# Kernel optimization log

Measured on AMD Instinct MI355X. Metric: run time of the kernel, lower is better.

## Reference

```python
import jax, jax.numpy as jnp
import numpy as np

NUM_HEADS = 8


def _proj(W, b, x):
    # x: [B, C, N] channel-wise 1x1 conv == matmul over channels
    return jnp.einsum('oc,bcn->bon', W, x) + b[None, :, None]


def setup_inputs() -> dict:
    key = jax.random.key(0)
    ks = jax.random.split(key, 8)
    B, C, H, W = 4, 512, 24, 24
    inp = {
        'feat0': jax.random.normal(ks[0], (B, C, H, W), jnp.float32),
        'feat1': jax.random.normal(ks[1], (B, C, H, W), jnp.float32),
        'feat2': jax.random.normal(ks[2], (B, C, H, W), jnp.float32),
        'Wq': jax.random.normal(ks[3], (C, C), jnp.float32) * 0.02,
        'bq': jnp.zeros((C,), jnp.float32),
        'Wk': jax.random.normal(ks[4], (C, C), jnp.float32) * 0.02,
        'bk': jnp.zeros((C,), jnp.float32),
        'Wv': jax.random.normal(ks[5], (C, C), jnp.float32) * 0.02,
        'bv': jnp.zeros((C,), jnp.float32),
        'Wo': jax.random.normal(ks[6], (C, C), jnp.float32) * 0.02,
        'bo': jnp.zeros((C,), jnp.float32),
    }
    return inp


def reference(feat0, feat1, feat2, Wq, bq, Wk, bk, Wv, bv, Wo, bo):
    feats = [feat0, feat1, feat2]
    B, C, H, W = feat0.shape
    h = NUM_HEADS
    d = C // h
    scale = d ** -0.5

    # Precompute K/V once per feature (the torch loop redundantly recomputes them;
    # the math is identical).
    flat = [f.reshape(B, C, H * W) for f in feats]
    K = jnp.concatenate([_proj(Wk, bk, x).reshape(B, h, d, -1) for x in flat], axis=-1)  # [B,h,d,KV]
    V = jnp.concatenate([_proj(Wv, bv, x).reshape(B, h, d, -1) for x in flat], axis=-1)  # [B,h,d,KV]

    outs = []
    for feat, x in zip(feats, flat):
        q = _proj(Wq, bq, x).reshape(B, h, d, H * W)  # [B,h,d,N]
        attn = jax.nn.softmax(jnp.einsum('bhdn,bhdm->bhnm', q, K) * scale, axis=-1)
        out = jnp.einsum('bhnm,bhdm->bhdn', attn, V).reshape(B, C, H * W)
        out = _proj(Wo, bo, out).reshape(B, C, H, W)
        outs.append(feat + out)
    return tuple(outs)
```

## Files before the change

kernel.cpp:

```cpp
#include <hip/hip_runtime.h>


using bf16x8 = __attribute__((ext_vector_type(8))) short;
using f32x4  = __attribute__((ext_vector_type(4))) float;
using f32x16 = __attribute__((ext_vector_type(16))) float;
using u32x4  = __attribute__((ext_vector_type(4))) unsigned int;
using u16x4  = __attribute__((ext_vector_type(4))) unsigned short;
using u16x8  = __attribute__((ext_vector_type(8))) unsigned short;

#define MFMA16(a, b, c) __builtin_amdgcn_mfma_f32_16x16x32_bf16((a), (b), (c), 0, 0, 0)
#define MFMA32(a, b, c) __builtin_amdgcn_mfma_f32_32x32x16_bf16((a), (b), (c), 0, 0, 0)

__device__ __forceinline__ unsigned short f2bf(float f) {
  unsigned int u = __float_as_uint(f);
  return (unsigned short)((u + 0x7fffu + ((u >> 16) & 1u)) >> 16);
}

__device__ __forceinline__ f32x16 zero16() {
  f32x16 z;
#pragma unroll
  for (int i = 0; i < 16; ++i) z[i] = 0.f;
  return z;
}

__device__ __forceinline__ void gload_lds16(const void* g, void* l) {
  __builtin_amdgcn_global_load_lds(
      (const __attribute__((address_space(1))) void*)g,
      (__attribute__((address_space(3))) void*)l, 16, 0, 0);
}

__global__ __launch_bounds__(256) void k_prep(
    const float* __restrict__ Wq, const float* __restrict__ Wk,
    const float* __restrict__ Wv, const float* __restrict__ Wo,
    const float* __restrict__ f0, const float* __restrict__ f1,
    const float* __restrict__ f2,
    unsigned short* __restrict__ Wf, unsigned short* __restrict__ Xf) {
  __shared__ unsigned short tile[64][65];
  const int bid = blockIdx.x;
  const int t = threadIdx.x;
  if (bid < 1024) {
    int idx = (bid * 256 + t) * 4;
    int p   = idx >> 18;
    int rem = idx & 262143;
    int o = rem >> 9, c0 = rem & 511;
    const float* s = p == 0 ? Wq : p == 1 ? Wk : p == 2 ? Wv : Wo;
    f32x4 v = *(const f32x4*)(s + rem);
    u16x4 pk;
    pk[0] = f2bf(v[0]); pk[1] = f2bf(v[1]); pk[2] = f2bf(v[2]); pk[3] = f2bf(v[3]);
    int mt = o >> 6, fr = (o & 63) >> 4, lr = o & 15;
    int ks = c0 >> 5, lg = (c0 & 31) >> 3, j0 = c0 & 7;
    size_t off = (size_t)((((p * 8 + mt) * 16 + ks) * 4 + fr)) * 512 +
                 (lg * 16 + lr) * 8 + j0;
    *(u16x4*)(Wf + off) = pk;
    return;
  }
  const int id = bid - 1024;
  const int nt = id % 9;
  const int ct = (id / 9) % 8;
  const int z  = id / 72;
  const int b = z / 3, f = z % 3;
  const float* src = (f == 0 ? f0 : f == 1 ? f1 : f2) + b * (512 * 576);

#pragma unroll
  for (int i = 0; i < 16; ++i) {
    int idx = i * 256 + t;
    int cc = idx >> 6, nn = idx & 63;
    tile[cc][nn] = f2bf(src[(ct * 64 + cc) * 576 + nt * 64 + nn]);
  }
  __syncthreads();
  const int ntw = f * 9 + nt;
#pragma unroll
  for (int i = 0; i < 4; ++i) {
    int slot = i * 256 + t;
    int nn = slot >> 4, cq = slot & 15;
    int cl = cq * 4;
    int c  = ct * 64 + cl;
    int fc = nn >> 4, lr = nn & 15;
    int ks = c >> 5, lg = (c & 31) >> 3, j0 = c & 7;
    u16x4 pk;
    pk[0] = tile[cl][nn]; pk[1] = tile[cl + 1][nn];
    pk[2] = tile[cl + 2][nn]; pk[3] = tile[cl + 3][nn];
    size_t off = (size_t)((((b * 27 + ntw) * 16 + ks) * 4 + fc)) * 512 +
                 (lg * 16 + lr) * 8 + j0;
    *(u16x4*)(Xf + off) = pk;
  }
}

__global__ __launch_bounds__(256) void k_gemm_qkv(
    const unsigned short* __restrict__ Wf, const unsigned short* __restrict__ Xf,
    const float* __restrict__ bq, const float* __restrict__ bk,
    const float* __restrict__ bv,
    unsigned short* __restrict__ Qf, unsigned short* __restrict__ Kf,
    unsigned short* __restrict__ Vf) {
  const int id = blockIdx.x;
  const int xcd = id & 7, s = id >> 3;
  const int b = xcd >> 1, par = xcd & 1;
  const int p = s / 54, bx = (s % 54) * 2 + par;
  const int t = threadIdx.x, w = t >> 6, l = t & 63, lg = l >> 4, lr = l & 15;
  const int wid = bx * 4 + w;
  const int mt = wid / 54, rest = wid % 54;
  const int ntw = rest >> 1, half = rest & 1;
  const unsigned short* A = Wf + (size_t)(p * 8 + mt) * 16 * 2048 + l * 8;
  const unsigned short* B = Xf + (size_t)(b * 27 + ntw) * 16 * 2048 +
                            half * 1024 + l * 8;

  f32x4 acc[4][2];
#pragma unroll
  for (int fr = 0; fr < 4; ++fr)
#pragma unroll
    for (int fc = 0; fc < 2; ++fc) acc[fr][fc] = (f32x4){0.f, 0.f, 0.f, 0.f};

#pragma unroll 2
  for (int ks = 0; ks < 16; ++ks) {
    bf16x8 af[4], bfv[2];
#pragma unroll
    for (int fr = 0; fr < 4; ++fr)
      af[fr] = *(const bf16x8*)(A + ks * 2048 + fr * 512);
#pragma unroll
    for (int fc = 0; fc < 2; ++fc)
      bfv[fc] = *(const bf16x8*)(B + ks * 2048 + fc * 512);
#pragma unroll
    for (int fr = 0; fr < 4; ++fr)
#pragma unroll
      for (int fc = 0; fc < 2; ++fc)
        acc[fr][fc] = MFMA16(af[fr], bfv[fc], acc[fr][fc]);
  }

  const float* bias = p == 0 ? bq : p == 1 ? bk : bv;
  const int bh = b * 8 + mt;
  const int ck = ntw * 2 + half;
#pragma unroll
  for (int fr = 0; fr < 4; ++fr) {
    f32x4 b4 = *(const f32x4*)(bias + mt * 64 + fr * 16 + lg * 4);
#pragma unroll
    for (int fc = 0; fc < 2; ++fc) {
      if (p < 2) {
        unsigned short* outF = (p == 0) ? Qf : Kf;
        u16x4 pk;
#pragma unroll
        for (int r = 0; r < 4; ++r) {
          float v = acc[fr][fc][r] + b4[r];
          if (p == 0) v *= 0.18033688f;
          pk[r] = f2bf(v);
        }
        size_t off = ((size_t)bh * 54 + ck) * 2048 + fr * 512 +
                     ((lg >> 1) * 32 + fc * 16 + lr) * 8 + (lg & 1) * 4;
        *(u16x4*)(outF + off) = pk;
      } else {
        size_t base = ((size_t)bh * 54 + ck) * 2048 +
                      ((fr >> 1) * 2 + fc) * 512 +
                      (((lr >> 3) & 1) * 32 + (fr & 1) * 16 + lg * 4) * 8 +
                      (lr & 7);
#pragma unroll
        for (int r = 0; r < 4; ++r)
          Vf[base + r * 8] = f2bf(acc[fr][fc][r] + b4[r]);
      }
    }
  }
}

__global__ __launch_bounds__(128, 4) void k_attn(
    const unsigned short* __restrict__ Qf, const unsigned short* __restrict__ Kf,
    const unsigned short* __restrict__ Vf, unsigned short* __restrict__ Of) {
  const int id = blockIdx.x;
  const int xcd = id & 7, slot = id >> 3;
  const int bh = xcd * 4 + (slot / 27);
  const int g  = slot % 27;
  const int b = bh >> 3, h = bh & 7;
  const int t = threadIdx.x, w = t >> 6, l = t & 63;
  const int lr = l & 31, hi = l >> 5;
  const int qt = g * 2 + w;

  __shared__ unsigned short kv[2][4096];
  __shared__ float Obuf[2][32][68];
  __shared__ float Lbuf[2][32];

  const unsigned short* Qb = Qf + ((size_t)bh * 54 + qt) * 2048 + l * 8;
  bf16x8 bq[4];
#pragma unroll
  for (int kf = 0; kf < 4; ++kf) bq[kf] = *(const bf16x8*)(Qb + kf * 512);

  f32x16 oacc[2];
  oacc[0] = zero16(); oacc[1] = zero16();
  float ls = 0.f;

  const unsigned short* gsrc =
      (w == 0 ? Kf : Vf) + (size_t)bh * 54 * 2048 + l * 8;

#pragma unroll
  for (int s2 = 0; s2 < 4; ++s2)
    gload_lds16(gsrc + s2 * 512, (char*)&kv[0][w * 2048] + s2 * 1024);

  int cur = 0;
#pragma unroll 1
  for (int ck = 0; ck < 54; ++ck) {
    __syncthreads();
    if (ck + 1 < 54) {
      const unsigned short* gs = gsrc + (size_t)(ck + 1) * 2048;
#pragma unroll
      for (int s2 = 0; s2 < 4; ++s2)
        gload_lds16(gs + s2 * 512, (char*)&kv[cur ^ 1][w * 2048] + s2 * 1024);
    }

    const unsigned short* kc = &kv[cur][0];
    const unsigned short* vc = &kv[cur][2048];
    bf16x8 ak[4];
#pragma unroll
    for (int i = 0; i < 4; ++i) ak[i] = *(const bf16x8*)(kc + i * 512 + l * 8);

    f32x16 sA = zero16();
#pragma unroll
    for (int kf = 0; kf < 4; ++kf) sA = MFMA32(ak[kf], bq[kf], sA);

    bf16x8 vb[4];
#pragma unroll
    for (int i = 0; i < 4; ++i) vb[i] = *(const bf16x8*)(vc + i * 512 + l * 8);

    unsigned int W[8];
    float a0 = 0.f, a1 = 0.f;
#pragma unroll
    for (int u = 0; u < 8; ++u) {
      float e0, e1;
      asm("v_exp_f32 %0, %1" : "=v"(e0) : "v"(sA[2 * u]));
      asm("v_exp_f32 %0, %1" : "=v"(e1) : "v"(sA[2 * u + 1]));
      a0 += e0; a1 += e1;
      asm("v_cvt_pk_bf16_f32 %0, %1, %2" : "=v"(W[u]) : "v"(e0), "v"(e1));
    }
    ls += a0 + a1;

    unsigned int fw[2][4];
#pragma unroll
    for (int kf = 0; kf < 2; ++kf)
#pragma unroll
      for (int wd = 0; wd < 2; ++wd) {
        unsigned int lo  = W[4 * kf + wd];
        unsigned int hw  = W[4 * kf + 2 + wd];
        unsigned int pub = hi ? lo : hw;
        unsigned int rcv = (unsigned int)__shfl_xor((int)pub, 32, 64);
        fw[kf][wd]     = hi ? rcv : lo;
        fw[kf][2 + wd] = hi ? hw : rcv;
      }
    u32x4 w0, w1;
    w0[0] = fw[0][0]; w0[1] = fw[0][1]; w0[2] = fw[0][2]; w0[3] = fw[0][3];
    w1[0] = fw[1][0]; w1[1] = fw[1][1]; w1[2] = fw[1][2]; w1[3] = fw[1][3];
    bf16x8 pa0 = __builtin_bit_cast(bf16x8, w0);
    bf16x8 pa1 = __builtin_bit_cast(bf16x8, w1);

    oacc[0] = MFMA32(pa0, vb[0], oacc[0]);
    oacc[0] = MFMA32(pa1, vb[1], oacc[0]);
    oacc[1] = MFMA32(pa0, vb[2], oacc[1]);
    oacc[1] = MFMA32(pa1, vb[3], oacc[1]);

    cur ^= 1;
  }

  float lt = ls + __shfl_xor(ls, 32, 64);
  if (l < 32) Lbuf[w][lr] = lt;
#pragma unroll
  for (int dt = 0; dt < 2; ++dt)
#pragma unroll
    for (int r = 0; r < 16; ++r)
      Obuf[w][(r & 3) + 8 * (r >> 2) + 4 * hi][dt * 32 + lr] = oacc[dt][r];

  const int n = l >> 1, dh = l & 1;
  float linv = 1.0f / Lbuf[w][n];
#pragma unroll
  for (int part = 0; part < 4; ++part) {
    const int d0 = dh * 32 + part * 8;
    u16x8 o8;
#pragma unroll
    for (int i = 0; i < 8; ++i) o8[i] = f2bf(Obuf[w][n][d0 + i] * linv);
    size_t off = (size_t)((((b * 27 + (qt >> 1)) * 16 + h * 2 + (d0 >> 5)) * 4 +
                           (qt & 1) * 2 + (n >> 4))) * 512 +
                 ((d0 >> 3) & 3) * 128 + (n & 15) * 8;
    *(u16x8*)(Of + off) = o8;
  }
}

__global__ __launch_bounds__(256) void k_gemm_out(
    const unsigned short* __restrict__ Wf, const unsigned short* __restrict__ Of,
    const float* __restrict__ bo,
    const float* __restrict__ f0, const float* __restrict__ f1,
    const float* __restrict__ f2, float* __restrict__ out) {
  const int z = blockIdx.z, b = z / 3, f = z % 3;
  const int t = threadIdx.x, w = t >> 6, l = t & 63, lg = l >> 4, lr = l & 15;
  const int wid = blockIdx.x * 4 + w;
  const int mt = wid / 18, rest = wid % 18;
  const int ntw = rest >> 1, half = rest & 1;
  const int o0 = mt * 64;
  const unsigned short* A = Wf + (size_t)(3 * 8 + mt) * 16 * 2048 + l * 8;
  const unsigned short* B = Of + (size_t)(b * 27 + f * 9 + ntw) * 16 * 2048 +
                            half * 1024 + l * 8;

  f32x4 acc[4][2];
#pragma unroll
  for (int fr = 0; fr < 4; ++fr)
#pragma unroll
    for (int fc = 0; fc < 2; ++fc) acc[fr][fc] = (f32x4){0.f, 0.f, 0.f, 0.f};

#pragma unroll 2
  for (int ks = 0; ks < 16; ++ks) {
    bf16x8 af[4], bfv[2];
#pragma unroll
    for (int fr = 0; fr < 4; ++fr)
      af[fr] = *(const bf16x8*)(A + ks * 2048 + fr * 512);
#pragma unroll
    for (int fc = 0; fc < 2; ++fc)
      bfv[fc] = *(const bf16x8*)(B + ks * 2048 + fc * 512);
#pragma unroll
    for (int fr = 0; fr < 4; ++fr)
#pragma unroll
      for (int fc = 0; fc < 2; ++fc)
        acc[fr][fc] = MFMA16(af[fr], bfv[fc], acc[fr][fc]);
  }

  const float* ft = f == 0 ? f0 : f == 1 ? f1 : f2;
#pragma unroll
  for (int fr = 0; fr < 4; ++fr) {
    f32x4 b4 = *(const f32x4*)(bo + o0 + fr * 16 + lg * 4);
#pragma unroll
    for (int fc = 0; fc < 2; ++fc) {
      int ncol = ntw * 64 + half * 32 + fc * 16 + lr;
#pragma unroll
      for (int r = 0; r < 4; ++r) {
        int o = o0 + fr * 16 + lg * 4 + r;
        out[((f * 4 + b) * 512 + o) * 576 + ncol] =
            acc[fr][fc][r] + b4[r] + ft[(b * 512 + o) * 576 + ncol];
      }
    }
  }
}

extern "C" void kernel_launch(void* const* d_in, const int* in_sizes, int n_in,
                              void* d_out, int out_size, void* d_ws, size_t ws_size,
                              hipStream_t stream) {
  const float* f0 = (const float*)d_in[0];
  const float* f1 = (const float*)d_in[1];
  const float* f2 = (const float*)d_in[2];
  const float* Wq = (const float*)d_in[3];
  const float* bq = (const float*)d_in[4];
  const float* Wk = (const float*)d_in[5];
  const float* bk = (const float*)d_in[6];
  const float* Wv = (const float*)d_in[7];
  const float* bv = (const float*)d_in[8];
  const float* Wo = (const float*)d_in[9];
  const float* bo = (const float*)d_in[10];
  float* out = (float*)d_out;

  char* ws = (char*)d_ws;
  unsigned short* Wf = (unsigned short*)(ws);
  unsigned short* Xf = (unsigned short*)(ws + 2097152);
  unsigned short* Qf = (unsigned short*)(ws + 9175040);
  unsigned short* Kf = (unsigned short*)(ws + 16252928);
  unsigned short* Vf = (unsigned short*)(ws + 23330816);
  unsigned short* Of = Xf;

  k_prep<<<dim3(1888), 256, 0, stream>>>(Wq, Wk, Wv, Wo, f0, f1, f2, Wf, Xf);
  k_gemm_qkv<<<dim3(1296), 256, 0, stream>>>(Wf, Xf, bq, bk, bv, Qf, Kf, Vf);
  k_attn<<<dim3(864), 128, 0, stream>>>(Qf, Kf, Vf, Of);
  k_gemm_out<<<dim3(36, 1, 12), 256, 0, stream>>>(Wf, Of, bo, f0, f1, f2, out);
}
```

Before: 103.7 us.

## Split attention KV loop across two wave pairs and merge partial outputs

The attention kernel grows from 2 to 4 waves per block. Each query tile is now handled by two waves that take alternating KV chunks, which halves the serial loop length per wave. Partial O accumulators and row sums are combined through shared memory, reusing the KV buffer as scratch, and the final normalization and store are spread over all 256 threads. The aim is more parallelism and latency hiding per block. The cost is extra syncs, the reduction step and doubled LDS per block, which may reduce occupancy. The merge relies on the softmax having no running max, so partial sums add directly.

After: 94.09 us. 1.1x faster.

```diff
diff --git a/kernel.cpp b/kernel.cpp
--- a/kernel.cpp
+++ b/kernel.cpp
@@ -159,7 +159,7 @@
   }
 }
 
-__global__ __launch_bounds__(128, 4) void k_attn(
+__global__ __launch_bounds__(256, 4) void k_attn(
     const unsigned short* __restrict__ Qf, const unsigned short* __restrict__ Kf,
     const unsigned short* __restrict__ Vf, unsigned short* __restrict__ Of) {
   const int id = blockIdx.x;
@@ -169,11 +169,11 @@
   const int b = bh >> 3, h = bh & 7;
   const int t = threadIdx.x, w = t >> 6, l = t & 63;
   const int lr = l & 31, hi = l >> 5;
-  const int qt = g * 2 + w;
-
-  __shared__ unsigned short kv[2][4096];
-  __shared__ float Obuf[2][32][68];
-  __shared__ float Lbuf[2][32];
+  const int tile = w >> 1, par = w & 1;
+  const int qt = g * 2 + tile;
+
+  __shared__ __align__(16) unsigned short kv[2][8192];
+  __shared__ float Lbuf[2][2][32];
 
   const unsigned short* Qb = Qf + ((size_t)bh * 54 + qt) * 2048 + l * 8;
   bf16x8 bq[4];
@@ -185,25 +185,29 @@
   float ls = 0.f;
 
   const unsigned short* gsrc =
-      (w == 0 ? Kf : Vf) + (size_t)bh * 54 * 2048 + l * 8;
-
-#pragma unroll
-  for (int s2 = 0; s2 < 4; ++s2)
-    gload_lds16(gsrc + s2 * 512, (char*)&kv[0][w * 2048] + s2 * 1024);
+      ((w & 1) ? Vf : Kf) + (size_t)bh * 54 * 2048 + l * 8;
+  const int soff = w >> 1;
+
+  {
+    const unsigned short* gs = gsrc + (size_t)soff * 2048;
+#pragma unroll
+    for (int s2 = 0; s2 < 4; ++s2)
+      gload_lds16(gs + s2 * 512, (char*)&kv[0][w * 2048] + s2 * 1024);
+  }
 
   int cur = 0;
 #pragma unroll 1
-  for (int ck = 0; ck < 54; ++ck) {
+  for (int r = 0; r < 27; ++r) {
     __syncthreads();
-    if (ck + 1 < 54) {
-      const unsigned short* gs = gsrc + (size_t)(ck + 1) * 2048;
+    if (r + 1 < 27) {
+      const unsigned short* gs = gsrc + (size_t)(2 * (r + 1) + soff) * 2048;
 #pragma unroll
       for (int s2 = 0; s2 < 4; ++s2)
         gload_lds16(gs + s2 * 512, (char*)&kv[cur ^ 1][w * 2048] + s2 * 1024);
     }
 
-    const unsigned short* kc = &kv[cur][0];
-    const unsigned short* vc = &kv[cur][2048];
+    const unsigned short* kc = &kv[cur][(par * 2) * 2048];
+    const unsigned short* vc = &kv[cur][(par * 2 + 1) * 2048];
     bf16x8 ak[4];
 #pragma unroll
     for (int i = 0; i < 4; ++i) ak[i] = *(const bf16x8*)(kc + i * 512 + l * 8);
@@ -255,23 +259,39 @@
   }
 
   float lt = ls + __shfl_xor(ls, 32, 64);
-  if (l < 32) Lbuf[w][lr] = lt;
-#pragma unroll
-  for (int dt = 0; dt < 2; ++dt)
-#pragma unroll
-    for (int r = 0; r < 16; ++r)
-      Obuf[w][(r & 3) + 8 * (r >> 2) + 4 * hi][dt * 32 + lr] = oacc[dt][r];
-
-  const int n = l >> 1, dh = l & 1;
-  float linv = 1.0f / Lbuf[w][n];
-#pragma unroll
-  for (int part = 0; part < 4; ++part) {
-    const int d0 = dh * 32 + part * 8;
+  __syncthreads();
+  float (*Obuf)[32][68] = (float (*)[32][68])kv;
+  if (par == 0) {
+#pragma unroll
+    for (int dt = 0; dt < 2; ++dt)
+#pragma unroll
+      for (int r = 0; r < 16; ++r)
+        Obuf[tile][(r & 3) + 8 * (r >> 2) + 4 * hi][dt * 32 + lr] = oacc[dt][r];
+    if (l < 32) Lbuf[tile][0][lr] = lt;
+  }
+  __syncthreads();
+  if (par == 1) {
+#pragma unroll
+    for (int dt = 0; dt < 2; ++dt)
+#pragma unroll
+      for (int r = 0; r < 16; ++r)
+        Obuf[tile][(r & 3) + 8 * (r >> 2) + 4 * hi][dt * 32 + lr] += oacc[dt][r];
+    if (l < 32) Lbuf[tile][1][lr] = lt;
+  }
+  __syncthreads();
+
+  const int tl2 = t >> 7, tt = t & 127;
+  const int n = tt >> 2, dq = tt & 3;
+  const int qts = g * 2 + tl2;
+  float linv = 1.0f / (Lbuf[tl2][0][n] + Lbuf[tl2][1][n]);
+#pragma unroll
+  for (int part = 0; part < 2; ++part) {
+    const int d0 = dq * 16 + part * 8;
     u16x8 o8;
 #pragma unroll
-    for (int i = 0; i < 8; ++i) o8[i] = f2bf(Obuf[w][n][d0 + i] * linv);
-    size_t off = (size_t)((((b * 27 + (qt >> 1)) * 16 + h * 2 + (d0 >> 5)) * 4 +
-                           (qt & 1) * 2 + (n >> 4))) * 512 +
+    for (int i = 0; i < 8; ++i) o8[i] = f2bf(Obuf[tl2][n][d0 + i] * linv);
+    size_t off = (size_t)((((b * 27 + (qts >> 1)) * 16 + h * 2 + (d0 >> 5)) * 4 +
+                           (qts & 1) * 2 + (n >> 4))) * 512 +
                  ((d0 >> 3) & 3) * 128 + (n & 15) * 8;
     *(u16x8*)(Of + off) = o8;
   }
@@ -357,6 +377,6 @@
 
   k_prep<<<dim3(1888), 256, 0, stream>>>(Wq, Wk, Wv, Wo, f0, f1, f2, Wf, Xf);
   k_gemm_qkv<<<dim3(1296), 256, 0, stream>>>(Wf, Xf, bq, bk, bv, Qf, Kf, Vf);
-  k_attn<<<dim3(864), 128, 0, stream>>>(Qf, Kf, Vf, Of);
+  k_attn<<<dim3(864), 256, 0, stream>>>(Qf, Kf, Vf, Of);
   k_gemm_out<<<dim3(36, 1, 12), 256, 0, stream>>>(Wf, Of, bo, f0, f1, f2, out);
 }
```
